# Performance work log

Measured on AMD Instinct MI355X. Metric: run time of the kernel, lower is better.

## Reference

```python
import math
import jax, jax.numpy as jnp
import numpy as np

C = 8.0  # decay constant from __init__
_MIN_RAD, _MAX_RAD = 0.9, 0.999


def block_diag_linear(x, w):
    # x: (B,T,D), w: (H, bs, bs) with D = H*bs
    B, T, D = x.shape
    H, bs, _ = w.shape
    xh = x.reshape(B, T, H, bs)
    return jnp.einsum('bthd,hde->bthe', xh, w).reshape(B, T, D)


def linear_scan(a, b):
    # h_t = a_t * h_{t-1} + b_t, h_{-1}=0, via associative scan:
    # (a1,b1) o (a2,b2) = (a1*a2, a2*b1 + b2)
    def op(l, r):
        a1, b1 = l
        a2, b2 = r
        return (a1 * a2, a2 * b1 + b2)
    return jax.lax.associative_scan(op, (a, b), axis=1)[1]


def setup_inputs() -> dict:
    key = jax.random.key(0)
    k1, k2, k3, k4 = jax.random.split(key, 4)
    B, T, D, H = 4, 4096, 1024, 8
    bs = D // H
    x = jax.random.normal(k1, (B, T, D), dtype=jnp.float32)
    std = 1.0 / math.sqrt(bs)
    w_in = jax.random.normal(k2, (H, bs, bs), dtype=jnp.float32) * std
    w_a = jax.random.normal(k3, (H, bs, bs), dtype=jnp.float32) * std
    # a_param init: softplus^{-1} of uniform in [-log(max_rad)/c, -log(min_rad)/c]
    sp = jax.random.uniform(k4, (D,), dtype=jnp.float32,
                            minval=-math.log(_MAX_RAD) / C,
                            maxval=-math.log(_MIN_RAD) / C)
    a_param = jnp.log(jnp.exp(sp) - 1.0 + 1e-8)
    return {"x": x, "a_param": a_param, "w_in": w_in, "w_a": w_a}


def reference(x, a_param, w_in, w_a):
    # RG-LRU forward with h_prev = None
    gate_x = jax.nn.sigmoid(block_diag_linear(x, w_in))  # input gate i_t
    gate_a = jax.nn.sigmoid(block_diag_linear(x, w_a))   # recurrence gate r_t
    log_a = -C * jax.nn.softplus(a_param) * gate_a       # (B,T,D)
    a = jnp.exp(log_a)
    multiplier = jnp.sqrt(1.0 - jnp.exp(2.0 * log_a))    # sqrt(1 - a^2)
    b = multiplier * (gate_x * x)
    y = linear_scan(a, b)                                 # (B,T,D)
    h_last = y[:, -1, :]
    return y, h_last
```

## Files before the change

kernel.cpp:

```cpp
#include <hip/hip_runtime.h>

#define B_ 4
#define T_ 4096
#define D_ 1024
#define H_ 8

typedef unsigned short u16;
typedef unsigned int u32;
typedef __attribute__((ext_vector_type(8))) short s16x8;
typedef __attribute__((ext_vector_type(4))) float f32x4;

#define LOG2E 1.4426950408889634f

__device__ __forceinline__ float ex2(float x){
#if __has_builtin(__builtin_amdgcn_exp2f)
  return __builtin_amdgcn_exp2f(x);
#else
  return exp2f(x);
#endif
}
__device__ __forceinline__ float rcpf(float x){
#if __has_builtin(__builtin_amdgcn_rcpf)
  return __builtin_amdgcn_rcpf(x);
#else
  return __fdividef(1.0f, x);
#endif
}
__device__ __forceinline__ u16 f2bf(float f){
  union { float f; u32 i; } v; v.f = f;
  u32 i = v.i;
  return (u16)((i + 0x7FFFu + ((i >> 16) & 1u)) >> 16);
}
__device__ __forceinline__ float sigf(float z){
  return rcpf(1.0f + ex2(-LOG2E * z));
}
__device__ __forceinline__ s16x8 cvt8(float4 a, float4 b){
  s16x8 r;
  r[0] = (short)(__float_as_uint(a.x) >> 16);
  r[1] = (short)(__float_as_uint(a.y) >> 16);
  r[2] = (short)(__float_as_uint(a.z) >> 16);
  r[3] = (short)(__float_as_uint(a.w) >> 16);
  r[4] = (short)(__float_as_uint(b.x) >> 16);
  r[5] = (short)(__float_as_uint(b.y) >> 16);
  r[6] = (short)(__float_as_uint(b.z) >> 16);
  r[7] = (short)(__float_as_uint(b.w) >> 16);
  return r;
}

__global__ __launch_bounds__(256) void k0_transpose(const float* __restrict__ w_in,
                                                    const float* __restrict__ w_a,
                                                    u16* __restrict__ wt){
  __shared__ float ls[128][132];
  const int blk = blockIdx.x;
  const float* src = (blk < 8 ? w_in : w_a) + (size_t)(blk & 7) * 128 * 128;
  u16* dst = wt + (size_t)blk * 128 * 128;
  const int tid = threadIdx.x;
  const int r0 = tid >> 5;
  const int c0 = (tid & 31) * 4;
  #pragma unroll
  for (int it = 0; it < 16; ++it){
    int r = r0 + it * 8;
    *(float4*)(&ls[r][c0]) = *(const float4*)(src + r * 128 + c0);
  }
  __syncthreads();
  #pragma unroll
  for (int it = 0; it < 16; ++it){
    int e = r0 + it * 8;
    ushort4 u;
    u.x = f2bf(ls[c0 + 0][e]);
    u.y = f2bf(ls[c0 + 1][e]);
    u.z = f2bf(ls[c0 + 2][e]);
    u.w = f2bf(ls[c0 + 3][e]);
    *(ushort4*)(dst + e * 128 + c0) = u;
  }
}

__global__ __launch_bounds__(256, 1) void k1_persist(
    const float* __restrict__ x, const float* __restrict__ a_param,
    const u16* __restrict__ wt, float* __restrict__ y_out,
    float* __restrict__ hlast)
{
  __shared__ float waveC[2][4][16][2];

  const int b = blockIdx.x;
  const int h = b & 7;
  const int batch = (b >> 3) & 3;
  const int cg = b >> 5;
  const int tid = threadIdx.x;
  const int w = tid >> 6;
  const int lane = tid & 63;
  const int q = lane >> 4, l = lane & 15;
  const int col = l;
  const int hcol = h * 128 + cg * 16 + col;

  const float asp = 8.0f * log1pf(__expf(a_param[hcol]));

  s16x8 bI[4], bA[4];
  {
    const u16* wb = wt + (size_t)(h * 128 + cg * 16 + col) * 128 + q * 8;
    #pragma unroll
    for (int kb = 0; kb < 4; ++kb){
      bI[kb] = *(const s16x8*)(wb + kb * 32);
      bA[kb] = *(const s16x8*)(wb + 8 * 128 * 128 + kb * 32);
    }
  }

  const float* pA0 = x + (size_t)(batch * T_ + w * 32 + l) * D_ + h * 128;
  const float* pA1 = pA0 + 16 * D_;

  float4 A0a[4][2], A1a[4][2], A0b[4][2], A1b[4][2];
  #pragma unroll
  for (int kb = 0; kb < 4; ++kb){
    const int ko = kb * 32 + q * 8;
    A0a[kb][0] = *(const float4*)(pA0 + ko);
    A0a[kb][1] = *(const float4*)(pA0 + ko + 4);
    A1a[kb][0] = *(const float4*)(pA1 + ko);
    A1a[kb][1] = *(const float4*)(pA1 + ko + 4);
  }
  pA0 += 128 * D_; pA1 += 128 * D_;

  float hin = 0.0f;

  auto tile_step = [&](float4 (&CA0)[4][2], float4 (&CA1)[4][2],
                       float4 (&NA0)[4][2], float4 (&NA1)[4][2], int tt)
  {
    const int mb = batch * T_ + tt * 128;
    float xv[2][4];
    {
      const float* xp = x + (size_t)(mb + w * 32 + q * 4) * D_ + hcol;
      #pragma unroll
      for (int mt = 0; mt < 2; ++mt)
        #pragma unroll
        for (int r = 0; r < 4; ++r)
          xv[mt][r] = xp[(size_t)(mt * 16 + r) * D_];
    }
    if (tt + 1 < 32){
      #pragma unroll
      for (int kb = 0; kb < 4; ++kb){
        const int ko = kb * 32 + q * 8;
        NA0[kb][0] = *(const float4*)(pA0 + ko);
        NA0[kb][1] = *(const float4*)(pA0 + ko + 4);
        NA1[kb][0] = *(const float4*)(pA1 + ko);
        NA1[kb][1] = *(const float4*)(pA1 + ko + 4);
      }
      pA0 += 128 * D_; pA1 += 128 * D_;
    }
    f32x4 accX[2], accG[2];
    accX[0] = (f32x4)0.0f; accX[1] = (f32x4)0.0f;
    accG[0] = (f32x4)0.0f; accG[1] = (f32x4)0.0f;
    #pragma unroll
    for (int kb = 0; kb < 4; ++kb){
      s16x8 a0 = cvt8(CA0[kb][0], CA0[kb][1]);
      s16x8 a1 = cvt8(CA1[kb][0], CA1[kb][1]);
      accX[0] = __builtin_amdgcn_mfma_f32_16x16x32_bf16(a0, bI[kb], accX[0], 0, 0, 0);
      accX[1] = __builtin_amdgcn_mfma_f32_16x16x32_bf16(a1, bI[kb], accX[1], 0, 0, 0);
      accG[0] = __builtin_amdgcn_mfma_f32_16x16x32_bf16(a0, bA[kb], accG[0], 0, 0, 0);
      accG[1] = __builtin_amdgcn_mfma_f32_16x16x32_bf16(a1, bA[kb], accG[1], 0, 0, 0);
    }
    float av[2][4], bv[2][4];
    #pragma unroll
    for (int mt = 0; mt < 2; ++mt){
      #pragma unroll
      for (int r = 0; r < 4; ++r){
        float gx = sigf(accX[mt][r]);
        float ga = sigf(accG[mt][r]);
        float la = -asp * ga;
        float a  = ex2(LOG2E * la);
        float mult = sqrtf(fmaxf(1.0f - a * a, 0.0f));
        av[mt][r] = a;
        bv[mt][r] = mult * gx * xv[mt][r];
      }
    }
    float preA[2], preY[2];
    float S0A = 1.0f, S0Y = 0.0f, WA = 1.0f, WY = 0.0f;
    #pragma unroll
    for (int mt = 0; mt < 2; ++mt){
      float a0 = av[mt][0], a1 = av[mt][1], a2 = av[mt][2], a3 = av[mt][3];
      float b0 = bv[mt][0], b1 = bv[mt][1], b2 = bv[mt][2], b3 = bv[mt][3];
      float TA = (a0 * a1) * (a2 * a3);
      float TY = fmaf(a3, fmaf(a2, fmaf(a1, b0, b1), b2), b3);
      float QA0 = __shfl(TA, l,      64), QY0 = __shfl(TY, l,      64);
      float QA1 = __shfl(TA, l + 16, 64), QY1 = __shfl(TY, l + 16, 64);
      float QA2 = __shfl(TA, l + 32, 64), QY2 = __shfl(TY, l + 32, 64);
      float QA3 = __shfl(TA, l + 48, 64), QY3 = __shfl(TY, l + 48, 64);
      float P1A = QA0,       P1Y = QY0;
      float P2A = P1A * QA1, P2Y = fmaf(QA1, P1Y, QY1);
      float P3A = P2A * QA2, P3Y = fmaf(QA2, P2Y, QY2);
      float QpA = (q == 0) ? 1.0f : ((q == 1) ? P1A : ((q == 2) ? P2A : P3A));
      float QpY = (q == 0) ? 0.0f : ((q == 1) ? P1Y : ((q == 2) ? P2Y : P3Y));
      float S16A = P3A * QA3, S16Y = fmaf(QA3, P3Y, QY3);
      preA[mt] = ((mt == 0) ? 1.0f : S0A) * QpA;
      preY[mt] = fmaf(QpA, ((mt == 0) ? 0.0f : S0Y), QpY);
      if (mt == 0){ S0A = S16A; S0Y = S16Y; }
      else { WA = S0A * S16A; WY = fmaf(S16A, S0Y, S16Y); }
    }
    if (lane < 16){
      waveC[tt & 1][w][col][0] = WA;
      waveC[tt & 1][w][col][1] = WY;
    }
    __syncthreads();
    float wpA = 1.0f, wpY = 0.0f, tAg = 1.0f, tYg = 0.0f;
    #pragma unroll
    for (int s = 0; s < 4; ++s){
      if (s == w){ wpA = tAg; wpY = tYg; }
      float cA = waveC[tt & 1][s][col][0];
      float cY = waveC[tt & 1][s][col][1];
      tYg = fmaf(cA, tYg, cY); tAg *= cA;
    }
    float hpre = fmaf(wpA, hin, wpY);
    #pragma unroll
    for (int mt = 0; mt < 2; ++mt){
      float v = fmaf(preA[mt], hpre, preY[mt]);
      float* yp = y_out + (size_t)(mb + w * 32 + mt * 16 + q * 4) * D_ + hcol;
      #pragma unroll
      for (int r = 0; r < 4; ++r){
        v = fmaf(av[mt][r], v, bv[mt][r]);
        yp[(size_t)r * D_] = v;
      }
    }
    hin = fmaf(tAg, hin, tYg);
  };

  for (int t = 0; t < 32; t += 2){
    tile_step(A0a, A1a, A0b, A1b, t);
    tile_step(A0b, A1b, A0a, A1a, t + 1);
  }

  if (tid < 16)
    hlast[batch * D_ + h * 128 + cg * 16 + tid] = hin;
}

extern "C" void kernel_launch(void* const* d_in, const int* in_sizes, int n_in,
                              void* d_out, int out_size, void* d_ws, size_t ws_size,
                              hipStream_t stream) {
  const float* x    = (const float*)d_in[0];
  const float* ap   = (const float*)d_in[1];
  const float* w_in = (const float*)d_in[2];
  const float* w_a  = (const float*)d_in[3];
  float* y = (float*)d_out;
  float* hlast = y + (size_t)B_ * T_ * D_;

  u16* wt = (u16*)d_ws;

  k0_transpose<<<16, 256, 0, stream>>>(w_in, w_a, wt);
  k1_persist<<<256, 256, 0, stream>>>(x, ap, wt, y, hlast);
}
```

Before: 188.4 us.

## Split each 128-row tile across eight waves of sixteen rows

The persistent scan kernel now launches 512 threads per block instead of 256, so each of eight waves handles 16 timesteps per 128-row tile instead of 32. The x values used for the b term are now software-prefetched alongside the MFMA operands. The aim is more waves in flight to hide global-load latency and shorter per-wave dependency chains, in exchange for a longer serial cross-wave combine through shared memory after each barrier.

```diff
diff --git a/kernel.cpp b/kernel.cpp
--- a/kernel.cpp
+++ b/kernel.cpp
@@ -75,12 +75,12 @@
   }
 }
 
-__global__ __launch_bounds__(256, 1) void k1_persist(
+__global__ __launch_bounds__(512, 2) void k1_persist(
     const float* __restrict__ x, const float* __restrict__ a_param,
     const u16* __restrict__ wt, float* __restrict__ y_out,
     float* __restrict__ hlast)
 {
-  __shared__ float waveC[2][4][16][2];
+  __shared__ float waveC[2][8][16][2];
 
   const int b = blockIdx.x;
   const int h = b & 7;
@@ -105,125 +105,95 @@
     }
   }
 
-  const float* pA0 = x + (size_t)(batch * T_ + w * 32 + l) * D_ + h * 128;
-  const float* pA1 = pA0 + 16 * D_;
-
-  float4 A0a[4][2], A1a[4][2], A0b[4][2], A1b[4][2];
+  const float* pA = x + (size_t)(batch * T_ + w * 16 + l) * D_ + h * 128;
+  const float* xp = x + (size_t)(batch * T_ + w * 16 + q * 4) * D_ + hcol;
+
+  float4 Aa[4][2], Ab[4][2];
+  float xva[4], xvb[4];
   #pragma unroll
   for (int kb = 0; kb < 4; ++kb){
     const int ko = kb * 32 + q * 8;
-    A0a[kb][0] = *(const float4*)(pA0 + ko);
-    A0a[kb][1] = *(const float4*)(pA0 + ko + 4);
-    A1a[kb][0] = *(const float4*)(pA1 + ko);
-    A1a[kb][1] = *(const float4*)(pA1 + ko + 4);
-  }
-  pA0 += 128 * D_; pA1 += 128 * D_;
+    Aa[kb][0] = *(const float4*)(pA + ko);
+    Aa[kb][1] = *(const float4*)(pA + ko + 4);
+  }
+  #pragma unroll
+  for (int r = 0; r < 4; ++r) xva[r] = xp[(size_t)r * D_];
+  pA += 128 * D_; xp += 128 * D_;
 
   float hin = 0.0f;
 
-  auto tile_step = [&](float4 (&CA0)[4][2], float4 (&CA1)[4][2],
-                       float4 (&NA0)[4][2], float4 (&NA1)[4][2], int tt)
+  auto tile_step = [&](float4 (&CA)[4][2], float4 (&NA)[4][2],
+                       float (&cxv)[4], float (&nxv)[4], int tt)
   {
     const int mb = batch * T_ + tt * 128;
-    float xv[2][4];
-    {
-      const float* xp = x + (size_t)(mb + w * 32 + q * 4) * D_ + hcol;
-      #pragma unroll
-      for (int mt = 0; mt < 2; ++mt)
-        #pragma unroll
-        for (int r = 0; r < 4; ++r)
-          xv[mt][r] = xp[(size_t)(mt * 16 + r) * D_];
-    }
     if (tt + 1 < 32){
       #pragma unroll
       for (int kb = 0; kb < 4; ++kb){
         const int ko = kb * 32 + q * 8;
-        NA0[kb][0] = *(const float4*)(pA0 + ko);
-        NA0[kb][1] = *(const float4*)(pA0 + ko + 4);
-        NA1[kb][0] = *(const float4*)(pA1 + ko);
-        NA1[kb][1] = *(const float4*)(pA1 + ko + 4);
+        NA[kb][0] = *(const float4*)(pA + ko);
+        NA[kb][1] = *(const float4*)(pA + ko + 4);
       }
-      pA0 += 128 * D_; pA1 += 128 * D_;
-    }
-    f32x4 accX[2], accG[2];
-    accX[0] = (f32x4)0.0f; accX[1] = (f32x4)0.0f;
-    accG[0] = (f32x4)0.0f; accG[1] = (f32x4)0.0f;
+      #pragma unroll
+      for (int r = 0; r < 4; ++r) nxv[r] = xp[(size_t)r * D_];
+      pA += 128 * D_; xp += 128 * D_;
+    }
+    f32x4 accX = (f32x4)0.0f, accG = (f32x4)0.0f;
     #pragma unroll
     for (int kb = 0; kb < 4; ++kb){
-      s16x8 a0 = cvt8(CA0[kb][0], CA0[kb][1]);
-      s16x8 a1 = cvt8(CA1[kb][0], CA1[kb][1]);
-      accX[0] = __builtin_amdgcn_mfma_f32_16x16x32_bf16(a0, bI[kb], accX[0], 0, 0, 0);
-      accX[1] = __builtin_amdgcn_mfma_f32_16x16x32_bf16(a1, bI[kb], accX[1], 0, 0, 0);
-      accG[0] = __builtin_amdgcn_mfma_f32_16x16x32_bf16(a0, bA[kb], accG[0], 0, 0, 0);
-      accG[1] = __builtin_amdgcn_mfma_f32_16x16x32_bf16(a1, bA[kb], accG[1], 0, 0, 0);
-    }
-    float av[2][4], bv[2][4];
-    #pragma unroll
-    for (int mt = 0; mt < 2; ++mt){
-      #pragma unroll
-      for (int r = 0; r < 4; ++r){
-        float gx = sigf(accX[mt][r]);
-        float ga = sigf(accG[mt][r]);
-        float la = -asp * ga;
-        float a  = ex2(LOG2E * la);
-        float mult = sqrtf(fmaxf(1.0f - a * a, 0.0f));
-        av[mt][r] = a;
-        bv[mt][r] = mult * gx * xv[mt][r];
-      }
-    }
-    float preA[2], preY[2];
-    float S0A = 1.0f, S0Y = 0.0f, WA = 1.0f, WY = 0.0f;
-    #pragma unroll
-    for (int mt = 0; mt < 2; ++mt){
-      float a0 = av[mt][0], a1 = av[mt][1], a2 = av[mt][2], a3 = av[mt][3];
-      float b0 = bv[mt][0], b1 = bv[mt][1], b2 = bv[mt][2], b3 = bv[mt][3];
-      float TA = (a0 * a1) * (a2 * a3);
-      float TY = fmaf(a3, fmaf(a2, fmaf(a1, b0, b1), b2), b3);
-      float QA0 = __shfl(TA, l,      64), QY0 = __shfl(TY, l,      64);
-      float QA1 = __shfl(TA, l + 16, 64), QY1 = __shfl(TY, l + 16, 64);
-      float QA2 = __shfl(TA, l + 32, 64), QY2 = __shfl(TY, l + 32, 64);
-      float QA3 = __shfl(TA, l + 48, 64), QY3 = __shfl(TY, l + 48, 64);
-      float P1A = QA0,       P1Y = QY0;
-      float P2A = P1A * QA1, P2Y = fmaf(QA1, P1Y, QY1);
-      float P3A = P2A * QA2, P3Y = fmaf(QA2, P2Y, QY2);
-      float QpA = (q == 0) ? 1.0f : ((q == 1) ? P1A : ((q == 2) ? P2A : P3A));
-      float QpY = (q == 0) ? 0.0f : ((q == 1) ? P1Y : ((q == 2) ? P2Y : P3Y));
-      float S16A = P3A * QA3, S16Y = fmaf(QA3, P3Y, QY3);
-      preA[mt] = ((mt == 0) ? 1.0f : S0A) * QpA;
-      preY[mt] = fmaf(QpA, ((mt == 0) ? 0.0f : S0Y), QpY);
-      if (mt == 0){ S0A = S16A; S0Y = S16Y; }
-      else { WA = S0A * S16A; WY = fmaf(S16A, S0Y, S16Y); }
-    }
+      s16x8 a0 = cvt8(CA[kb][0], CA[kb][1]);
+      accX = __builtin_amdgcn_mfma_f32_16x16x32_bf16(a0, bI[kb], accX, 0, 0, 0);
+      accG = __builtin_amdgcn_mfma_f32_16x16x32_bf16(a0, bA[kb], accG, 0, 0, 0);
+    }
+    float av[4], bv[4];
+    #pragma unroll
+    for (int r = 0; r < 4; ++r){
+      float gx = sigf(accX[r]);
+      float ga = sigf(accG[r]);
+      float la = -asp * ga;
+      float a  = ex2(LOG2E * la);
+      float mult = sqrtf(fmaxf(1.0f - a * a, 0.0f));
+      av[r] = a;
+      bv[r] = mult * gx * cxv[r];
+    }
+    float TA = (av[0] * av[1]) * (av[2] * av[3]);
+    float TY = fmaf(av[3], fmaf(av[2], fmaf(av[1], bv[0], bv[1]), bv[2]), bv[3]);
+    float QA0 = __shfl(TA, l,      64), QY0 = __shfl(TY, l,      64);
+    float QA1 = __shfl(TA, l + 16, 64), QY1 = __shfl(TY, l + 16, 64);
+    float QA2 = __shfl(TA, l + 32, 64), QY2 = __shfl(TY, l + 32, 64);
+    float QA3 = __shfl(TA, l + 48, 64), QY3 = __shfl(TY, l + 48, 64);
+    float P1A = QA0,       P1Y = QY0;
+    float P2A = P1A * QA1, P2Y = fmaf(QA1, P1Y, QY1);
+    float P3A = P2A * QA2, P3Y = fmaf(QA2, P2Y, QY2);
+    float QpA = (q == 0) ? 1.0f : ((q == 1) ? P1A : ((q == 2) ? P2A : P3A));
+    float QpY = (q == 0) ? 0.0f : ((q == 1) ? P1Y : ((q == 2) ? P2Y : P3Y));
+    float SA = P3A * QA3, SY = fmaf(QA3, P3Y, QY3);
     if (lane < 16){
-      waveC[tt & 1][w][col][0] = WA;
-      waveC[tt & 1][w][col][1] = WY;
+      waveC[tt & 1][w][col][0] = SA;
+      waveC[tt & 1][w][col][1] = SY;
     }
     __syncthreads();
     float wpA = 1.0f, wpY = 0.0f, tAg = 1.0f, tYg = 0.0f;
     #pragma unroll
-    for (int s = 0; s < 4; ++s){
+    for (int s = 0; s < 8; ++s){
       if (s == w){ wpA = tAg; wpY = tYg; }
       float cA = waveC[tt & 1][s][col][0];
       float cY = waveC[tt & 1][s][col][1];
       tYg = fmaf(cA, tYg, cY); tAg *= cA;
     }
     float hpre = fmaf(wpA, hin, wpY);
-    #pragma unroll
-    for (int mt = 0; mt < 2; ++mt){
-      float v = fmaf(preA[mt], hpre, preY[mt]);
-      float* yp = y_out + (size_t)(mb + w * 32 + mt * 16 + q * 4) * D_ + hcol;
-      #pragma unroll
-      for (int r = 0; r < 4; ++r){
-        v = fmaf(av[mt][r], v, bv[mt][r]);
-        yp[(size_t)r * D_] = v;
-      }
+    float v = fmaf(QpA, hpre, QpY);
+    float* yp = y_out + (size_t)(mb + w * 16 + q * 4) * D_ + hcol;
+    #pragma unroll
+    for (int r = 0; r < 4; ++r){
+      v = fmaf(av[r], v, bv[r]);
+      yp[(size_t)r * D_] = v;
     }
     hin = fmaf(tAg, hin, tYg);
   };
 
   for (int t = 0; t < 32; t += 2){
-    tile_step(A0a, A1a, A0b, A1b, t);
-    tile_step(A0b, A1b, A0a, A1a, t + 1);
+    tile_step(Aa, Ab, xva, xvb, t);
+    tile_step(Ab, Aa, xvb, xva, t + 1);
   }
 
   if (tid < 16)
@@ -243,5 +213,5 @@
   u16* wt = (u16*)d_ws;
 
   k0_transpose<<<16, 256, 0, stream>>>(w_in, w_a, wt);
-  k1_persist<<<256, 256, 0, stream>>>(x, ap, wt, y, hlast);
-}
+  k1_persist<<<256, 512, 0, stream>>>(x, ap, wt, y, hlast);
+}
```

After: 199.6 us. +6.0%, slower.
